# Kernel optimization log

Hardware: AMD Instinct MI355X
Metric: run time of the kernel (lower is better)

The kernel has to match this reference:

```python
import jax, jax.numpy as jnp
import numpy as np

LN_EPS = 1e-5


def setup_inputs() -> dict:
    key = jax.random.key(0)
    k1, k2, k3 = jax.random.split(key, 3)
    N, E, D_IN, D_OUT = 50000, 500000, 128, 128
    x = jax.random.normal(k1, (N, D_IN), dtype=jnp.float32)
    edge_index = jax.random.randint(k2, (2, E), 0, N, dtype=jnp.int64)
    W = jax.random.normal(k3, (D_IN, D_OUT), dtype=jnp.float32) * (1.0 / np.sqrt(D_IN))
    b = jnp.zeros((D_OUT,), dtype=jnp.float32)
    ln_gamma = jnp.ones((D_OUT,), dtype=jnp.float32)
    ln_beta = jnp.zeros((D_OUT,), dtype=jnp.float32)
    return {"x": x, "edge_index": edge_index, "W": W, "b": b,
            "ln_gamma": ln_gamma, "ln_beta": ln_beta}


def reference(x, edge_index, W, b, ln_gamma, ln_beta):
    N = x.shape[0]
    # GCNConv: linear transform first (no fused bias; bias added after aggregation)
    h = x @ W  # [N, D_out]
    # add self-loops
    loops = jnp.arange(N, dtype=edge_index.dtype)
    src = jnp.concatenate([edge_index[0], loops])  # [E+N]
    dst = jnp.concatenate([edge_index[1], loops])  # [E+N]
    # symmetric normalization deg^{-1/2} (degree computed on dst, incl. self-loops)
    deg = jax.ops.segment_sum(jnp.ones(src.shape, dtype=h.dtype), dst, num_segments=N)
    dinv = jnp.where(deg > 0, jax.lax.rsqrt(deg), 0.0)
    norm = dinv[src] * dinv[dst]  # [E+N]
    # gather messages, scale, scatter-add to destinations
    msgs = h[src] * norm[:, None]  # [E+N, D_out]
    out = jax.ops.segment_sum(msgs, dst, num_segments=N) + b  # [N, D_out]
    # LayerNorm over features
    mu = out.mean(axis=-1, keepdims=True)
    var = out.var(axis=-1, keepdims=True)
    out = (out - mu) * jax.lax.rsqrt(var + LN_EPS) * ln_gamma + ln_beta
    # activation
    return jax.nn.relu(out)
```

## Files before the change

kernel.cpp:

```cpp
#include <hip/hip_runtime.h>
#include <math.h>

#define D 128
#define LN_EPS 1e-5f
#define BKT 64

__device__ __forceinline__ float bf_lo(unsigned u) {
    union { unsigned u; float f; } c; c.u = u << 16; return c.f;
}
__device__ __forceinline__ float bf_hi(unsigned u) {
    union { unsigned u; float f; } c; c.u = u & 0xffff0000u; return c.f;
}
__device__ __forceinline__ unsigned pack_bf2(float a, float b) {
    union { float f; unsigned u; } x, y; x.f = a; y.f = b;
    unsigned ua = x.u + (0x7fffu + ((x.u >> 16) & 1u));
    unsigned ub = y.u + (0x7fffu + ((y.u >> 16) & 1u));
    return (ua >> 16) | (ub & 0xffff0000u);
}

__global__ void gemm_kernel(const float* __restrict__ x, const float* __restrict__ W,
                            unsigned* __restrict__ h2, int N) {
    __shared__ float xs[64][D];
    int tid  = threadIdx.x;
    int row0 = blockIdx.x * 64;
#pragma unroll
    for (int i = 0; i < 8; ++i) {
        int idx = i * 256 + tid;
        int r   = idx >> 5;
        int c4  = idx & 31;
        float4 v = make_float4(0.f, 0.f, 0.f, 0.f);
        if (row0 + r < N) v = *(const float4*)&x[(size_t)(row0 + r) * D + c4 * 4];
        *(float4*)&xs[r][c4 * 4] = v;
    }
    __syncthreads();

    int cg    = tid & 31;
    int rbase = (tid >> 5) * 8;
    float4 acc[8];
#pragma unroll
    for (int i = 0; i < 8; ++i) acc[i] = make_float4(0.f, 0.f, 0.f, 0.f);

#pragma unroll 2
    for (int k = 0; k < D; k += 4) {
        float4 w0 = *(const float4*)&W[(k + 0) * D + cg * 4];
        float4 w1 = *(const float4*)&W[(k + 1) * D + cg * 4];
        float4 w2 = *(const float4*)&W[(k + 2) * D + cg * 4];
        float4 w3 = *(const float4*)&W[(k + 3) * D + cg * 4];
#pragma unroll
        for (int r = 0; r < 8; ++r) {
            float4 xv = *(const float4*)&xs[rbase + r][k];
            acc[r].x = fmaf(xv.x, w0.x, acc[r].x);
            acc[r].y = fmaf(xv.x, w0.y, acc[r].y);
            acc[r].z = fmaf(xv.x, w0.z, acc[r].z);
            acc[r].w = fmaf(xv.x, w0.w, acc[r].w);
            acc[r].x = fmaf(xv.y, w1.x, acc[r].x);
            acc[r].y = fmaf(xv.y, w1.y, acc[r].y);
            acc[r].z = fmaf(xv.y, w1.z, acc[r].z);
            acc[r].w = fmaf(xv.y, w1.w, acc[r].w);
            acc[r].x = fmaf(xv.z, w2.x, acc[r].x);
            acc[r].y = fmaf(xv.z, w2.y, acc[r].y);
            acc[r].z = fmaf(xv.z, w2.z, acc[r].z);
            acc[r].w = fmaf(xv.z, w2.w, acc[r].w);
            acc[r].x = fmaf(xv.w, w3.x, acc[r].x);
            acc[r].y = fmaf(xv.w, w3.y, acc[r].y);
            acc[r].z = fmaf(xv.w, w3.z, acc[r].z);
            acc[r].w = fmaf(xv.w, w3.w, acc[r].w);
        }
    }
#pragma unroll
    for (int r = 0; r < 8; ++r) {
        int row = row0 + rbase + r;
        if (row < N) {
            uint2 p = make_uint2(pack_bf2(acc[r].x, acc[r].y),
                                 pack_bf2(acc[r].z, acc[r].w));
            *(uint2*)&h2[(size_t)row * (D / 2) + cg * 2] = p;
        }
    }
}

__global__ void bucket_kernel(const int* __restrict__ src, const int* __restrict__ dst,
                              int* __restrict__ degi, int* __restrict__ bucket, int E) {
    int t  = blockIdx.x * blockDim.x + threadIdx.x;
    int e0 = t * 4;
    if (e0 + 3 < E) {
        int4 d4 = *(const int4*)&dst[e0];
        int4 s4 = *(const int4*)&src[e0];
        int p0 = atomicAdd(&degi[d4.x], 1);
        int p1 = atomicAdd(&degi[d4.y], 1);
        int p2 = atomicAdd(&degi[d4.z], 1);
        int p3 = atomicAdd(&degi[d4.w], 1);
        if (p0 < BKT) bucket[(size_t)d4.x * BKT + p0] = s4.x;
        if (p1 < BKT) bucket[(size_t)d4.y * BKT + p1] = s4.y;
        if (p2 < BKT) bucket[(size_t)d4.z * BKT + p2] = s4.z;
        if (p3 < BKT) bucket[(size_t)d4.w * BKT + p3] = s4.w;
    } else {
        for (int e = e0; e < E; ++e) {
            int d = dst[e];
            int p = atomicAdd(&degi[d], 1);
            if (p < BKT) bucket[(size_t)d * BKT + p] = src[e];
        }
    }
}

__global__ void gather_ln_kernel(const int* __restrict__ bucket, const int* __restrict__ degi,
                                 const unsigned* __restrict__ h2, const float* __restrict__ b,
                                 const float* __restrict__ g, const float* __restrict__ be,
                                 float* __restrict__ out, int N) {
    int row  = blockIdx.x * 4 + (threadIdx.x >> 6);
    int lane = threadIdx.x & 63;
    if (row >= N) return;
    int dg  = degi[row];
    int dgc = dg < BKT ? dg : BKT;
    float di = rsqrtf((float)dg + 1.0f);
    float sw = di * di;
    unsigned su = h2[(size_t)row * (D / 2) + lane];
    float acc0 = bf_lo(su) * sw;
    float acc1 = bf_hi(su) * sw;
    const int* bk = bucket + (size_t)row * BKT;
    int e = 0;
    for (; e + 3 < dgc; e += 4) {
        int s0 = bk[e], s1 = bk[e + 1], s2 = bk[e + 2], s3 = bk[e + 3];
        float w0 = rsqrtf((float)degi[s0] + 1.0f) * di;
        float w1 = rsqrtf((float)degi[s1] + 1.0f) * di;
        float w2 = rsqrtf((float)degi[s2] + 1.0f) * di;
        float w3 = rsqrtf((float)degi[s3] + 1.0f) * di;
        unsigned u0 = h2[(size_t)s0 * (D / 2) + lane];
        unsigned u1 = h2[(size_t)s1 * (D / 2) + lane];
        unsigned u2 = h2[(size_t)s2 * (D / 2) + lane];
        unsigned u3 = h2[(size_t)s3 * (D / 2) + lane];
        acc0 = fmaf(bf_lo(u0), w0, acc0);  acc1 = fmaf(bf_hi(u0), w0, acc1);
        acc0 = fmaf(bf_lo(u1), w1, acc0);  acc1 = fmaf(bf_hi(u1), w1, acc1);
        acc0 = fmaf(bf_lo(u2), w2, acc0);  acc1 = fmaf(bf_hi(u2), w2, acc1);
        acc0 = fmaf(bf_lo(u3), w3, acc0);  acc1 = fmaf(bf_hi(u3), w3, acc1);
    }
    for (; e < dgc; ++e) {
        int s = bk[e];
        float w = rsqrtf((float)degi[s] + 1.0f) * di;
        unsigned u = h2[(size_t)s * (D / 2) + lane];
        acc0 = fmaf(bf_lo(u), w, acc0);
        acc1 = fmaf(bf_hi(u), w, acc1);
    }
    float2 bb = *(const float2*)&b[lane * 2];
    float v0 = acc0 + bb.x;
    float v1 = acc1 + bb.y;
    float s = v0 + v1;
    float q = v0 * v0 + v1 * v1;
#pragma unroll
    for (int off = 32; off; off >>= 1) {
        s += __shfl_xor(s, off);
        q += __shfl_xor(q, off);
    }
    float mean = s * (1.0f / 128.0f);
    float var  = q * (1.0f / 128.0f) - mean * mean;
    float rstd = rsqrtf(var + LN_EPS);
    float2 gg = *(const float2*)&g[lane * 2];
    float2 eb = *(const float2*)&be[lane * 2];
    float y0 = (v0 - mean) * rstd * gg.x + eb.x;
    float y1 = (v1 - mean) * rstd * gg.y + eb.y;
    *(float2*)&out[(size_t)row * D + lane * 2] = make_float2(fmaxf(y0, 0.0f), fmaxf(y1, 0.0f));
}

extern "C" void kernel_launch(void* const* d_in, const int* in_sizes, int n_in,
                              void* d_out, int out_size, void* d_ws, size_t ws_size,
                              hipStream_t stream) {
    const float* x  = (const float*)d_in[0];
    const int*   ei = (const int*)d_in[1];
    const float* W  = (const float*)d_in[2];
    const float* b  = (const float*)d_in[3];
    const float* g  = (const float*)d_in[4];
    const float* be = (const float*)d_in[5];

    int N = in_sizes[0] / D;
    int E = in_sizes[1] / 2;
    const int* src = ei;
    const int* dst = ei + E;

    float* out = (float*)d_out;

    char* w = (char*)d_ws;
    unsigned* h2   = (unsigned*)w;            w += (size_t)N * (D / 2) * sizeof(unsigned);
    int*   degi    = (int*)w;                 w += (size_t)N * sizeof(int);
    int*   bucket  = (int*)w;                 w += (size_t)N * BKT * sizeof(int);

    hipMemsetAsync(degi, 0, (size_t)N * sizeof(int), stream);

    gemm_kernel  <<<(N + 63) / 64,          256, 0, stream>>>(x, W, h2, N);
    bucket_kernel<<<(E / 4 + 255) / 256 + 1, 256, 0, stream>>>(src, dst, degi, bucket, E);
    gather_ln_kernel<<<(N + 3) / 4,         256, 0, stream>>>(bucket, degi, h2,
                                                              b, g, be, out, N);
}
```

Before: 171.6 us.

## Pad degree counters to separate cache lines and precompute dinv in finalize kernel

Degree counters are spaced 32 ints apart, one per 128-byte line, so atomics on different nodes no longer contend on the same line. A new finalize kernel compacts the clamped degree and precomputes deg^-1/2 once per node, so the gather kernel loads dinv instead of computing rsqrt per edge. The bucket kernel now handles one edge per thread instead of four. The cost is a 6.4 MB memset, a strided read in finalize and one extra kernel launch.

```diff
diff --git a/kernel.cpp b/kernel.cpp
--- a/kernel.cpp
+++ b/kernel.cpp
@@ -4,6 +4,7 @@
 #define D 128
 #define LN_EPS 1e-5f
 #define BKT 64
+#define DSTRIDE 32
 
 __device__ __forceinline__ float bf_lo(unsigned u) {
     union { unsigned u; float f; } c; c.u = u << 16; return c.f;
@@ -79,39 +80,35 @@
 }
 
 __global__ void bucket_kernel(const int* __restrict__ src, const int* __restrict__ dst,
-                              int* __restrict__ degi, int* __restrict__ bucket, int E) {
-    int t  = blockIdx.x * blockDim.x + threadIdx.x;
-    int e0 = t * 4;
-    if (e0 + 3 < E) {
-        int4 d4 = *(const int4*)&dst[e0];
-        int4 s4 = *(const int4*)&src[e0];
-        int p0 = atomicAdd(&degi[d4.x], 1);
-        int p1 = atomicAdd(&degi[d4.y], 1);
-        int p2 = atomicAdd(&degi[d4.z], 1);
-        int p3 = atomicAdd(&degi[d4.w], 1);
-        if (p0 < BKT) bucket[(size_t)d4.x * BKT + p0] = s4.x;
-        if (p1 < BKT) bucket[(size_t)d4.y * BKT + p1] = s4.y;
-        if (p2 < BKT) bucket[(size_t)d4.z * BKT + p2] = s4.z;
-        if (p3 < BKT) bucket[(size_t)d4.w * BKT + p3] = s4.w;
-    } else {
-        for (int e = e0; e < E; ++e) {
-            int d = dst[e];
-            int p = atomicAdd(&degi[d], 1);
-            if (p < BKT) bucket[(size_t)d * BKT + p] = src[e];
-        }
+                              int* __restrict__ degp, int* __restrict__ bucket, int E) {
+    int e = blockIdx.x * blockDim.x + threadIdx.x;
+    if (e < E) {
+        int d = dst[e];
+        int p = atomicAdd(&degp[(size_t)d * DSTRIDE], 1);
+        if (p < BKT) bucket[(size_t)d * BKT + p] = src[e];
     }
 }
 
-__global__ void gather_ln_kernel(const int* __restrict__ bucket, const int* __restrict__ degi,
+__global__ void finalize_kernel(const int* __restrict__ degp, int* __restrict__ degc,
+                                float* __restrict__ dinv, int N) {
+    int i = blockIdx.x * blockDim.x + threadIdx.x;
+    if (i < N) {
+        int d = degp[(size_t)i * DSTRIDE];
+        degc[i] = d < BKT ? d : BKT;
+        dinv[i] = rsqrtf((float)d + 1.0f);
+    }
+}
+
+__global__ void gather_ln_kernel(const int* __restrict__ bucket, const int* __restrict__ degc,
+                                 const float* __restrict__ dinv,
                                  const unsigned* __restrict__ h2, const float* __restrict__ b,
                                  const float* __restrict__ g, const float* __restrict__ be,
                                  float* __restrict__ out, int N) {
     int row  = blockIdx.x * 4 + (threadIdx.x >> 6);
     int lane = threadIdx.x & 63;
     if (row >= N) return;
-    int dg  = degi[row];
-    int dgc = dg < BKT ? dg : BKT;
-    float di = rsqrtf((float)dg + 1.0f);
+    int dgc  = degc[row];
+    float di = dinv[row];
     float sw = di * di;
     unsigned su = h2[(size_t)row * (D / 2) + lane];
     float acc0 = bf_lo(su) * sw;
@@ -120,10 +117,10 @@
     int e = 0;
     for (; e + 3 < dgc; e += 4) {
         int s0 = bk[e], s1 = bk[e + 1], s2 = bk[e + 2], s3 = bk[e + 3];
-        float w0 = rsqrtf((float)degi[s0] + 1.0f) * di;
-        float w1 = rsqrtf((float)degi[s1] + 1.0f) * di;
-        float w2 = rsqrtf((float)degi[s2] + 1.0f) * di;
-        float w3 = rsqrtf((float)degi[s3] + 1.0f) * di;
+        float w0 = dinv[s0] * di;
+        float w1 = dinv[s1] * di;
+        float w2 = dinv[s2] * di;
+        float w3 = dinv[s3] * di;
         unsigned u0 = h2[(size_t)s0 * (D / 2) + lane];
         unsigned u1 = h2[(size_t)s1 * (D / 2) + lane];
         unsigned u2 = h2[(size_t)s2 * (D / 2) + lane];
@@ -135,7 +132,7 @@
     }
     for (; e < dgc; ++e) {
         int s = bk[e];
-        float w = rsqrtf((float)degi[s] + 1.0f) * di;
+        float w = dinv[s] * di;
         unsigned u = h2[(size_t)s * (D / 2) + lane];
         acc0 = fmaf(bf_lo(u), w, acc0);
         acc1 = fmaf(bf_hi(u), w, acc1);
@@ -179,13 +176,16 @@
 
     char* w = (char*)d_ws;
     unsigned* h2   = (unsigned*)w;            w += (size_t)N * (D / 2) * sizeof(unsigned);
-    int*   degi    = (int*)w;                 w += (size_t)N * sizeof(int);
+    int*   degp    = (int*)w;                 w += (size_t)N * DSTRIDE * sizeof(int);
+    int*   degc    = (int*)w;                 w += (size_t)N * sizeof(int);
+    float* dinv    = (float*)w;               w += (size_t)N * sizeof(float);
     int*   bucket  = (int*)w;                 w += (size_t)N * BKT * sizeof(int);
 
-    hipMemsetAsync(degi, 0, (size_t)N * sizeof(int), stream);
+    hipMemsetAsync(degp, 0, (size_t)N * DSTRIDE * sizeof(int), stream);
 
-    gemm_kernel  <<<(N + 63) / 64,          256, 0, stream>>>(x, W, h2, N);
-    bucket_kernel<<<(E / 4 + 255) / 256 + 1, 256, 0, stream>>>(src, dst, degi, bucket, E);
-    gather_ln_kernel<<<(N + 3) / 4,         256, 0, stream>>>(bucket, degi, h2,
-                                                              b, g, be, out, N);
+    gemm_kernel    <<<(N + 63) / 64,   256, 0, stream>>>(x, W, h2, N);
+    bucket_kernel  <<<(E + 255) / 256, 256, 0, stream>>>(src, dst, degp, bucket, E);
+    finalize_kernel<<<(N + 255) / 256, 256, 0, stream>>>(degp, degc, dinv, N);
+    gather_ln_kernel<<<(N + 3) / 4,    256, 0, stream>>>(bucket, degc, dinv, h2,
+                                                         b, g, be, out, N);
 }
```

Measured after the change: 171.2 us. No clear change (-0.2%).
